# Performance work log

Measured on AMD Instinct MI355X. Metric: run time of the kernel, lower is better.

The kernel has to match this reference:

```python
import jax, jax.numpy as jnp
import numpy as np

D_MODEL = 1024
H = 16
D_K = D_MODEL // H
D_FF = 4096
EPS = 1e-6


def setup_inputs() -> dict:
    key = jax.random.key(0)
    ks = jax.random.split(key, 12)
    B, S = 8, 1024
    s = 0.02
    inp = {
        "x": jax.random.normal(ks[0], (B, S, D_MODEL), dtype=jnp.float32),
        "src_mask": jnp.ones((B, 1, 1, S), dtype=jnp.int32),
        "wq": jax.random.normal(ks[1], (D_MODEL, D_MODEL), dtype=jnp.float32) * s,
        "bq": jnp.zeros((D_MODEL,), jnp.float32),
        "wk": jax.random.normal(ks[2], (D_MODEL, D_MODEL), dtype=jnp.float32) * s,
        "bk": jnp.zeros((D_MODEL,), jnp.float32),
        "wv": jax.random.normal(ks[3], (D_MODEL, D_MODEL), dtype=jnp.float32) * s,
        "bv": jnp.zeros((D_MODEL,), jnp.float32),
        "wo": jax.random.normal(ks[4], (D_MODEL, D_MODEL), dtype=jnp.float32) * s,
        "bo": jnp.zeros((D_MODEL,), jnp.float32),
        "w1": jax.random.normal(ks[5], (D_FF, D_MODEL), dtype=jnp.float32) * s,
        "b1": jnp.zeros((D_FF,), jnp.float32),
        "w2": jax.random.normal(ks[6], (D_MODEL, D_FF), dtype=jnp.float32) * s,
        "b2": jnp.zeros((D_MODEL,), jnp.float32),
        "ln1_a": jnp.ones((1,), jnp.float32),
        "ln1_b": jnp.zeros((1,), jnp.float32),
        "ln2_a": jnp.ones((1,), jnp.float32),
        "ln2_b": jnp.zeros((1,), jnp.float32),
    }
    return inp


def _layernorm(x, alpha, bias):
    # matches torch: std with Bessel correction (ddof=1), eps added to std
    mean = jnp.mean(x, axis=-1, keepdims=True)
    std = jnp.std(x, axis=-1, keepdims=True, ddof=1)
    return (x - mean) / (std + EPS) * alpha + bias


def reference(x, src_mask, wq, bq, wk, bk, wv, bv, wo, bo, w1, b1, w2, b2,
              ln1_a, ln1_b, ln2_a, ln2_b):
    B, S, _ = x.shape
    # --- residual 1: self attention on pre-normed x ---
    n = _layernorm(x, ln1_a, ln1_b)
    q = n @ wq.T + bq
    # NOTE: the source has a bug: key and value are views of the *query*
    # projection (w_k/w_v outputs are computed but discarded). We reproduce it.
    _ = n @ wk.T + bk
    _ = n @ wv.T + bv
    qh = q.reshape(B, S, H, D_K).transpose(0, 2, 1, 3)  # [B,H,S,dk]
    kh = qh
    vh = qh
    scores = jnp.einsum('bhqd,bhkd->bhqk', qh, kh) / jnp.sqrt(jnp.float32(D_K))
    scores = jnp.where(src_mask == 0, jnp.float32(-1e9), scores)
    attn = jax.nn.softmax(scores, axis=-1)
    ctx = jnp.einsum('bhqk,bhkd->bhqd', attn, vh)
    ctx = ctx.transpose(0, 2, 1, 3).reshape(B, S, D_MODEL)
    x = x + (ctx @ wo.T + bo)
    # --- residual 2: feed-forward (intended ReLU MLP) ---
    n2 = _layernorm(x, ln2_a, ln2_b)
    h = jax.nn.relu(n2 @ w1.T + b1)
    x = x + (h @ w2.T + b2)
    return x
```

## Files before the change

### kernel.cpp

```cpp
#include <hip/hip_runtime.h>
#include <hip/hip_bf16.h>

typedef __attribute__((ext_vector_type(8))) short short8;
typedef __attribute__((ext_vector_type(4))) float f32x4;

#define MFMA16(a, b, c) __builtin_amdgcn_mfma_f32_16x16x32_bf16((a), (b), (c), 0, 0, 0)

__device__ __forceinline__ unsigned short f2bf(float f) {
  union { float f; unsigned int u; } v; v.f = f;
  return (unsigned short)((v.u + 0x7fffu + ((v.u >> 16) & 1u)) >> 16);
}

__device__ __forceinline__ void gload_lds16(const void* g, void* l) {
  __builtin_amdgcn_global_load_lds((__attribute__((address_space(1))) void*)g,
                                   (__attribute__((address_space(3))) void*)l,
                                   16, 0, 0);
}

struct CvtArgs {
  const float* s0; const float* s1; const float* s2; const float* s3;
  unsigned short* d0; unsigned short* d1; unsigned short* d2; unsigned short* d3;
};

__global__ __launch_bounds__(256) void cvt_weights(CvtArgs a) {
  const long N0 = 1048576, N1 = 1048576, N2 = 4194304;
  long i = ((long)blockIdx.x * 256 + threadIdx.x) * 4;
  const float* s; unsigned short* d; long off;
  if (i < N0)                { s = a.s0; d = a.d0; off = i; }
  else if (i < N0 + N1)      { s = a.s1; d = a.d1; off = i - N0; }
  else if (i < N0 + N1 + N2) { s = a.s2; d = a.d2; off = i - N0 - N1; }
  else                       { s = a.s3; d = a.d3; off = i - N0 - N1 - N2; }
  float4 v = *(const float4*)(s + off);
  ushort4 o;
  o.x = f2bf(v.x); o.y = f2bf(v.y); o.z = f2bf(v.z); o.w = f2bf(v.w);
  *(ushort4*)(d + off) = o;
}

__global__ __launch_bounds__(256) void ln_kernel(
    const float* __restrict__ x,
    const float* __restrict__ alpha, const float* __restrict__ beta,
    unsigned short* __restrict__ out) {
  const int row = blockIdx.x;
  const int tid = threadIdx.x;
  const float4 v = ((const float4*)(x + (size_t)row * 1024))[tid];
  float s  = v.x + v.y + v.z + v.w;
  float sq = v.x * v.x + v.y * v.y + v.z * v.z + v.w * v.w;
  #pragma unroll
  for (int d = 32; d >= 1; d >>= 1) {
    s  += __shfl_xor(s, d, 64);
    sq += __shfl_xor(sq, d, 64);
  }
  __shared__ float red[8];
  const int w = tid >> 6;
  if ((tid & 63) == 0) { red[w] = s; red[4 + w] = sq; }
  __syncthreads();
  s  = red[0] + red[1] + red[2] + red[3];
  sq = red[4] + red[5] + red[6] + red[7];
  const float mean = s * (1.f / 1024.f);
  float var = (sq - s * mean) * (1.f / 1023.f);
  var = fmaxf(var, 0.f);
  const float rs = alpha[0] / (sqrtf(var) + 1e-6f);
  const float bb = beta[0];
  ushort4 o;
  o.x = f2bf((v.x - mean) * rs + bb);
  o.y = f2bf((v.y - mean) * rs + bb);
  o.z = f2bf((v.z - mean) * rs + bb);
  o.w = f2bf((v.w - mean) * rs + bb);
  ((ushort4*)out)[(size_t)row * 256 + tid] = o;
}

template <int OUT_BF16, int RELU, int NF>
__global__ __launch_bounds__(512, 2) void gemm2ph(
    const unsigned short* __restrict__ A, int lda,
    const unsigned short* __restrict__ B, int ldb,
    const float* __restrict__ bias,
    const float* __restrict__ residual,
    void* __restrict__ Cout,
    int M, int N, int K, float cscale, int nbx) {
  __shared__ __align__(16) unsigned short lds[32768 + NF * 8192];
  const int NT = K >> 6;
  const int tid = threadIdx.x;
  const int w = tid >> 6, lane = tid & 63;
  const int cpx = gridDim.x >> 3;
  const int id = (blockIdx.x & 7) * cpx + (blockIdx.x >> 3);
  const int bx = id % nbx, by = id / nbx;
  const int row0 = by * 256, col0 = bx * (NF * 64);
  const int wr128 = (w >> 2) * 128, wcN = (w & 3) * (NF * 16);
  const int lq = lane & 15, g = lane >> 4, g4 = g * 4;
  const int strow = tid >> 3;
  const int sunit8 = ((tid & 7) ^ (strow & 7)) * 8;

  const unsigned short* Asrc = A + (size_t)(row0 + strow) * lda + sunit8;
  const unsigned short* Bsrc = B + (size_t)(col0 + strow) * ldb + sunit8;

  auto stage = [&](int buf, int tt) {
    unsigned short* Ad = lds + buf * 16384 + w * 512;
    unsigned short* Bd = lds + 32768 + buf * (NF * 4096) + w * 512;
    #pragma unroll
    for (int c = 0; c < 4; ++c)
      gload_lds16(Asrc + (size_t)(c * 64) * lda + tt * 64, Ad + c * 4096);
    #pragma unroll
    for (int c = 0; c < NF; ++c)
      gload_lds16(Bsrc + (size_t)(c * 64) * ldb + tt * 64, Bd + c * 4096);
  };

  f32x4 acc[8][NF] = {};

  stage(0, 0);
  asm volatile("s_waitcnt vmcnt(0)" ::: "memory");
  __builtin_amdgcn_s_barrier();
  int buf = 0;

  for (int t = 0; t < NT; ++t) {
    if (t + 1 < NT) stage(buf ^ 1, t + 1);
    const unsigned short* Ab = lds + buf * 16384;
    const unsigned short* Bb = lds + 32768 + buf * (NF * 4096);
    #pragma unroll
    for (int kk = 0; kk < 2; ++kk) {
      short8 af[8], bf[NF];
      #pragma unroll
      for (int m = 0; m < 8; ++m) {
        const int r = wr128 + m * 16 + lq;
        af[m] = *(const short8*)(Ab + r * 64 + (((kk * 4 + g) ^ (r & 7)) << 3));
      }
      #pragma unroll
      for (int n = 0; n < NF; ++n) {
        const int r = wcN + n * 16 + lq;
        bf[n] = *(const short8*)(Bb + r * 64 + (((kk * 4 + g) ^ (r & 7)) << 3));
      }
      __builtin_amdgcn_s_setprio(1);
      #pragma unroll
      for (int m = 0; m < 8; ++m)
        #pragma unroll
        for (int n = 0; n < NF; ++n)
          acc[m][n] = MFMA16(af[m], bf[n], acc[m][n]);
      __builtin_amdgcn_s_setprio(0);
    }
    if (t + 1 < NT) {
      asm volatile("s_waitcnt vmcnt(0)" ::: "memory");
      __builtin_amdgcn_s_barrier();
      buf ^= 1;
    }
  }

  float bv[NF];
  #pragma unroll
  for (int n = 0; n < NF; ++n) bv[n] = bias[col0 + wcN + n * 16 + lq];

  if (OUT_BF16) {
    const int CW = NF * 64 + 4;
    unsigned short* cbuf = lds;
    __syncthreads();
    #pragma unroll
    for (int p = 0; p < 2; ++p) {
      if ((w >> 2) == p) {
        #pragma unroll
        for (int m = 0; m < 8; ++m)
          #pragma unroll
          for (int n = 0; n < NF; ++n)
            #pragma unroll
            for (int r = 0; r < 4; ++r) {
              float v = (acc[m][n][r] + bv[n]) * cscale;
              if (RELU) v = fmaxf(v, 0.f);
              cbuf[(m * 16 + g4 + r) * CW + wcN + n * 16 + lq] = f2bf(v);
            }
      }
      __syncthreads();
      #pragma unroll
      for (int i = 0; i < 2 * NF; ++i) {
        const int un = i * 512 + tid;
        const int row = un / (8 * NF);
        const int cu = un % (8 * NF);
        const short8 vv = *(const short8*)&cbuf[row * CW + cu * 8];
        *(short8*)((unsigned short*)Cout + (size_t)(row0 + p * 128 + row) * N + col0 + cu * 8) = vv;
      }
      __syncthreads();
    }
  } else {
    #pragma unroll
    for (int n = 0; n < NF; ++n) {
      const int col = col0 + wcN + n * 16 + lq;
      #pragma unroll
      for (int m = 0; m < 8; ++m) {
        #pragma unroll
        for (int r = 0; r < 4; ++r) {
          const int row = row0 + wr128 + m * 16 + g4 + r;
          float v = (acc[m][n][r] + bv[n]) * cscale;
          if (RELU) v = fmaxf(v, 0.f);
          const size_t idx = (size_t)row * N + col;
          if (residual) v += residual[idx];
          ((float*)Cout)[idx] = v;
        }
      }
    }
  }
}

__global__ __launch_bounds__(256) void transpose_q(
    const unsigned short* __restrict__ q, unsigned short* __restrict__ qT) {
  const int st = blockIdx.x, bh = blockIdx.y;
  const int b = bh >> 4, h = bh & 15;
  __shared__ __align__(16) unsigned short tile[64][80];
  const int tid = threadIdx.x;
  const unsigned short* src = q + ((size_t)(b * 1024 + st * 64)) * 1024 + h * 64;
  #pragma unroll
  for (int j = 0; j < 2; ++j) {
    const int u = tid + j * 256;
    const int sl = u >> 3, d8 = (u & 7) * 8;
    *(short8*)&tile[sl][d8] = *(const short8*)&src[(size_t)sl * 1024 + d8];
  }
  __syncthreads();
  unsigned short* dst = qT + ((size_t)(bh * 64)) * 1024 + st * 64;
  #pragma unroll
  for (int j = 0; j < 2; ++j) {
    const int u = tid + j * 256;
    const int dl = u >> 3, s8 = (u & 7) * 8;
    short8 o;
    #pragma unroll
    for (int i = 0; i < 8; ++i) o[i] = (short)tile[s8 + i][dl];
    *(short8*)&dst[(size_t)dl * 1024 + s8] = o;
  }
}

__global__ __launch_bounds__(256) void attn_kernel(
    const unsigned short* __restrict__ q,
    const unsigned short* __restrict__ qT,
    const int* __restrict__ mask,
    unsigned short* __restrict__ ctx) {
  __shared__ __align__(16) unsigned short Ks[2][64 * 64];
  __shared__ __align__(16) unsigned short Vs[2][64 * 64];
  __shared__ int allmask;
  const int id = blockIdx.x;
  const int bh = ((id & 7) << 4) + (id >> 6);
  const int qt = (id >> 3) & 7;
  const int b = bh >> 4, h = bh & 15;
  const int tid = threadIdx.x, w = tid >> 6, lane = tid & 63;
  const int lq = lane & 15;
  const int g = lane >> 4;
  const int lk8 = g * 8;
  const int swz = lane & 7;
  const int q0 = qt * 128 + w * 32;
  const size_t qbase = (size_t)b * (1024 * 1024) + h * 64;
  const size_t qTb = (size_t)bh * 64 * 1024;
  const int srow = lane >> 3;
  const int su = (lane & 7) ^ srow;
  const size_t ksrc = qbase + (size_t)(w * 16 + srow) * 1024 + su * 8;
  const size_t vsrc = qTb + (size_t)(w * 16 + srow) * 1024 + su * 8;
  const float RS = 2.3548202f;

  auto stage = [&](int bufi, int kt) {
    char* Kd = (char*)Ks[bufi] + w * 2048;
    char* Vd = (char*)Vs[bufi] + w * 2048;
    gload_lds16(q + ksrc + (size_t)(kt * 64) * 1024, Kd);
    gload_lds16(q + ksrc + (size_t)(kt * 64 + 8) * 1024, Kd + 1024);
    gload_lds16(qT + vsrc + kt * 64, Vd);
    gload_lds16(qT + vsrc + (size_t)8 * 1024 + kt * 64, Vd + 1024);
  };

  const int* mrow = mask + b * 1024;
  if (tid == 0) allmask = 1;
  int mp = 1;
  #pragma unroll
  for (int i = 0; i < 4; ++i) mp &= (mrow[tid + i * 256] != 0);
  stage(0, 0);
  __syncthreads();
  if (!__all(mp) && lane == 0) atomicAnd(&allmask, 0);
  asm volatile("s_waitcnt vmcnt(0)" ::: "memory");
  __syncthreads();
  const bool fullmask = (allmask != 0);

  short8 qa[2][2];
  #pragma unroll
  for (int qf = 0; qf < 2; ++qf)
    #pragma unroll
    for (int kk = 0; kk < 2; ++kk)
      qa[qf][kk] = *(const short8*)&q[qbase + (size_t)(q0 + qf * 16 + lq) * 1024 + kk * 32 + lk8];

  short8 ones;
  #pragma unroll
  for (int i = 0; i < 8; ++i) ones[i] = (short)0x3F80;

  float mrun[2] = {-1e30f, -1e30f};
  f32x4 lacc[2] = {};
  f32x4 Oa[2][4];
  #pragma unroll
  for (int mf = 0; mf < 2; ++mf)
    #pragma unroll
    for (int nf = 0; nf < 4; ++nf) Oa[mf][nf] = (f32x4){0.f, 0.f, 0.f, 0.f};

  int cur = 0;

  for (int kt = 0; kt < 16; ++kt) {
    const int k0 = kt * 64;
    if (kt < 15) stage(cur ^ 1, kt + 1);
    const char* Kb = (const char*)Ks[cur];
    const char* Vb = (const char*)Vs[cur];
    f32x4 s[2][4];
    #pragma unroll
    for (int qf = 0; qf < 2; ++qf)
      #pragma unroll
      for (int kf = 0; kf < 4; ++kf) s[qf][kf] = (f32x4){0.f, 0.f, 0.f, 0.f};
    #pragma unroll
    for (int kf = 0; kf < 4; ++kf) {
      const char* kr = Kb + (kf * 16 + lq) * 128;
      const short8 ka0 = *(const short8*)(kr + (((g) ^ swz) << 4));
      const short8 ka1 = *(const short8*)(kr + (((4 + g) ^ swz) << 4));
      s[0][kf] = MFMA16(ka0, qa[0][0], s[0][kf]);
      s[0][kf] = MFMA16(ka1, qa[0][1], s[0][kf]);
      s[1][kf] = MFMA16(ka0, qa[1][0], s[1][kf]);
      s[1][kf] = MFMA16(ka1, qa[1][1], s[1][kf]);
    }
    float pmax[2] = {-1e30f, -1e30f};
    if (fullmask) {
      #pragma unroll
      for (int kf = 0; kf < 4; ++kf)
        #pragma unroll
        for (int qf = 0; qf < 2; ++qf)
          #pragma unroll
          for (int r = 0; r < 4; ++r)
            pmax[qf] = fmaxf(pmax[qf], s[qf][kf][r]);
    } else {
      #pragma unroll
      for (int kf = 0; kf < 4; ++kf) {
        const int4 mv = *(const int4*)&mrow[k0 + kf * 16 + g * 4];
        float madd[4];
        madd[0] = mv.x ? 0.f : -1e9f; madd[1] = mv.y ? 0.f : -1e9f;
        madd[2] = mv.z ? 0.f : -1e9f; madd[3] = mv.w ? 0.f : -1e9f;
        #pragma unroll
        for (int qf = 0; qf < 2; ++qf)
          #pragma unroll
          for (int r = 0; r < 4; ++r) {
            const float v = s[qf][kf][r] + madd[r];
            s[qf][kf][r] = v;
            pmax[qf] = fmaxf(pmax[qf], v);
          }
      }
    }
    #pragma unroll
    for (int qf = 0; qf < 2; ++qf) {
      pmax[qf] = fmaxf(pmax[qf], __shfl_xor(pmax[qf], 16, 64));
      pmax[qf] = fmaxf(pmax[qf], __shfl_xor(pmax[qf], 32, 64));
    }
    const int ok = (pmax[0] <= mrun[0] + 8.f) && (pmax[1] <= mrun[1] + 8.f);
    if (!__all(ok)) {
      float corr[2];
      #pragma unroll
      for (int qf = 0; qf < 2; ++qf) {
        const float mn = fmaxf(mrun[qf], pmax[qf]);
        corr[qf] = exp2f(mrun[qf] - mn);
        mrun[qf] = mn;
      }
      #pragma unroll
      for (int mf = 0; mf < 2; ++mf)
        #pragma unroll
        for (int r = 0; r < 4; ++r) {
          const float c = __shfl(corr[mf], g * 4 + r, 64);
          lacc[mf][r] *= c;
          #pragma unroll
          for (int nf = 0; nf < 4; ++nf) Oa[mf][nf][r] *= c;
        }
    }
    unsigned int E[2][4], O[2][4];
    #pragma unroll
    for (int qf = 0; qf < 2; ++qf) {
      #pragma unroll
      for (int kf = 0; kf < 4; ++kf) {
        float p0 = exp2f(s[qf][kf][0] - mrun[qf]);
        float p1 = exp2f(s[qf][kf][1] - mrun[qf]);
        float p2 = exp2f(s[qf][kf][2] - mrun[qf]);
        float p3 = exp2f(s[qf][kf][3] - mrun[qf]);
        asm("v_cvt_pk_bf16_f32 %0, %1, %2" : "=v"(E[qf][kf]) : "v"(p0), "v"(p1));
        asm("v_cvt_pk_bf16_f32 %0, %1, %2" : "=v"(O[qf][kf]) : "v"(p2), "v"(p3));
      }
    }
    short8 pa[2][2];
    #pragma unroll
    for (int qf = 0; qf < 2; ++qf) {
      #pragma unroll
      for (int ks = 0; ks < 2; ++ks) {
        unsigned int e0 = E[qf][2 * ks], e1 = E[qf][2 * ks + 1];
        unsigned int o0 = O[qf][2 * ks], o1 = O[qf][2 * ks + 1];
        asm("v_permlane32_swap_b32 %0, %1" : "+v"(e0), "+v"(e1));
        asm("v_permlane16_swap_b32 %0, %1" : "+v"(e0), "+v"(e1));
        asm("v_permlane32_swap_b32 %0, %1" : "+v"(o0), "+v"(o1));
        asm("v_permlane16_swap_b32 %0, %1" : "+v"(o0), "+v"(o1));
        union { unsigned int u[4]; short8 s8; } pw;
        pw.u[0] = e0; pw.u[1] = o0; pw.u[2] = e1; pw.u[3] = o1;
        pa[qf][ks] = pw.s8;
      }
    }
    #pragma unroll
    for (int ks = 0; ks < 2; ++ks) {
      #pragma unroll
      for (int nf = 0; nf < 4; ++nf) {
        const short8 vb = *(const short8*)(Vb + (nf * 16 + lq) * 128 + (((4 * ks + g) ^ swz) << 4));
        Oa[0][nf] = MFMA16(pa[0][ks], vb, Oa[0][nf]);
        Oa[1][nf] = MFMA16(pa[1][ks], vb, Oa[1][nf]);
      }
      lacc[0] = MFMA16(pa[0][ks], ones, lacc[0]);
      lacc[1] = MFMA16(pa[1][ks], ones, lacc[1]);
    }
    __syncthreads();
    cur ^= 1;
  }
  #pragma unroll
  for (int mf = 0; mf < 2; ++mf) {
    #pragma unroll
    for (int r = 0; r < 4; ++r) {
      const float linv = RS / lacc[mf][r];
      const int row = q0 + mf * 16 + g * 4 + r;
      #pragma unroll
      for (int nf = 0; nf < 4; ++nf) {
        const int col = h * 64 + nf * 16 + lq;
        ctx[((size_t)b * 1024 + row) * 1024 + col] = f2bf(Oa[mf][nf][r] * linv);
      }
    }
  }
}

extern "C" void kernel_launch(void* const* d_in, const int* in_sizes, int n_in,
                              void* d_out, int out_size, void* d_ws, size_t ws_size,
                              hipStream_t stream) {
  const float* x    = (const float*)d_in[0];
  const int*   mask = (const int*)d_in[1];
  const float* wq   = (const float*)d_in[2];
  const float* bq   = (const float*)d_in[3];
  const float* wo   = (const float*)d_in[8];
  const float* bo   = (const float*)d_in[9];
  const float* w1   = (const float*)d_in[10];
  const float* b1   = (const float*)d_in[11];
  const float* w2   = (const float*)d_in[12];
  const float* b2   = (const float*)d_in[13];
  const float* ln1a = (const float*)d_in[14];
  const float* ln1b = (const float*)d_in[15];
  const float* ln2a = (const float*)d_in[16];
  const float* ln2b = (const float*)d_in[17];
  float* out = (float*)d_out;

  char* ws = (char*)d_ws;
  unsigned short* wq_b  = (unsigned short*)(ws);
  unsigned short* wo_b  = (unsigned short*)(ws + (2l << 20));
  unsigned short* w1_b  = (unsigned short*)(ws + (4l << 20));
  unsigned short* w2_b  = (unsigned short*)(ws + (12l << 20));
  unsigned short* n_b   = (unsigned short*)(ws + (20l << 20));
  unsigned short* q_b   = (unsigned short*)(ws + (36l << 20));
  unsigned short* qT_b  = (unsigned short*)(ws + (52l << 20));
  unsigned short* ctx_b = (unsigned short*)(ws + (68l << 20));
  unsigned short* h_b   = (unsigned short*)(ws + (84l << 20));

  const float SQRT_SC = 0.42466090f;

  CvtArgs ca{wq, wo, w1, w2, wq_b, wo_b, w1_b, w2_b};
  cvt_weights<<<10240, 256, 0, stream>>>(ca);
  ln_kernel<<<8192, 256, 0, stream>>>(x, ln1a, ln1b, n_b);
  gemm2ph<1, 0, 2><<<256, 512, 0, stream>>>(n_b, 1024, wq_b, 1024, bq, nullptr, q_b, 8192, 1024, 1024, SQRT_SC, 8);
  transpose_q<<<dim3(16, 128), 256, 0, stream>>>(q_b, qT_b);
  attn_kernel<<<1024, 256, 0, stream>>>(q_b, qT_b, mask, ctx_b);
  gemm2ph<0, 0, 2><<<256, 512, 0, stream>>>(ctx_b, 1024, wo_b, 1024, bo, x, out, 8192, 1024, 1024, 1.0f, 8);
  ln_kernel<<<8192, 256, 0, stream>>>(out, ln2a, ln2b, n_b);
  gemm2ph<1, 1, 4><<<512, 512, 0, stream>>>(n_b, 1024, w1_b, 1024, b1, nullptr, h_b, 8192, 4096, 1024, 1.0f, 16);
  gemm2ph<0, 0, 2><<<256, 512, 0, stream>>>(h_b, 4096, w2_b, 4096, b2, out, out, 8192, 1024, 4096, 1.0f, 8);
}
```

Before: 323.4 us.

## Switch GEMMs to triple-buffered LDS pipeline with fixed 256x128 tiles

Replaces the double-buffered GEMM with a three-stage LDS ring: two tiles are prefetched ahead, and each iteration waits only on the older outstanding loads (vmcnt(6)) instead of draining all of them. The tile width is fixed at 128 columns, so the FFN up-projection now uses 256x128 tiles across 1024 blocks instead of 256x256 tiles across 512. LDS use rises to about 144KB per block and launch bounds drop to one block per CU. Hiding more global-load latency comes at the cost of occupancy and less B-tile reuse in the wide GEMM.

```diff
diff --git a/kernel.cpp b/kernel.cpp
--- a/kernel.cpp
+++ b/kernel.cpp
@@ -69,23 +69,23 @@
   ((ushort4*)out)[(size_t)row * 256 + tid] = o;
 }
 
-template <int OUT_BF16, int RELU, int NF>
-__global__ __launch_bounds__(512, 2) void gemm2ph(
+template <int OUT_BF16, int RELU>
+__global__ __launch_bounds__(512, 1) void gemm3(
     const unsigned short* __restrict__ A, int lda,
     const unsigned short* __restrict__ B, int ldb,
     const float* __restrict__ bias,
     const float* __restrict__ residual,
     void* __restrict__ Cout,
     int M, int N, int K, float cscale, int nbx) {
-  __shared__ __align__(16) unsigned short lds[32768 + NF * 8192];
+  __shared__ __align__(16) unsigned short lds[3 * 24576];
   const int NT = K >> 6;
   const int tid = threadIdx.x;
   const int w = tid >> 6, lane = tid & 63;
   const int cpx = gridDim.x >> 3;
   const int id = (blockIdx.x & 7) * cpx + (blockIdx.x >> 3);
   const int bx = id % nbx, by = id / nbx;
-  const int row0 = by * 256, col0 = bx * (NF * 64);
-  const int wr128 = (w >> 2) * 128, wcN = (w & 3) * (NF * 16);
+  const int row0 = by * 256, col0 = bx * 128;
+  const int wr128 = (w >> 2) * 128, wcN = (w & 3) * 32;
   const int lq = lane & 15, g = lane >> 4, g4 = g * 4;
   const int strow = tid >> 3;
   const int sunit8 = ((tid & 7) ^ (strow & 7)) * 8;
@@ -93,38 +93,46 @@
   const unsigned short* Asrc = A + (size_t)(row0 + strow) * lda + sunit8;
   const unsigned short* Bsrc = B + (size_t)(col0 + strow) * ldb + sunit8;
 
-  auto stage = [&](int buf, int tt) {
-    unsigned short* Ad = lds + buf * 16384 + w * 512;
-    unsigned short* Bd = lds + 32768 + buf * (NF * 4096) + w * 512;
+  auto stage = [&](int bufi, int tt) {
+    unsigned short* Ad = lds + bufi * 24576 + w * 512;
+    unsigned short* Bd = lds + bufi * 24576 + 16384 + w * 512;
     #pragma unroll
     for (int c = 0; c < 4; ++c)
       gload_lds16(Asrc + (size_t)(c * 64) * lda + tt * 64, Ad + c * 4096);
     #pragma unroll
-    for (int c = 0; c < NF; ++c)
+    for (int c = 0; c < 2; ++c)
       gload_lds16(Bsrc + (size_t)(c * 64) * ldb + tt * 64, Bd + c * 4096);
   };
 
-  f32x4 acc[8][NF] = {};
+  f32x4 acc[8][2] = {};
 
   stage(0, 0);
-  asm volatile("s_waitcnt vmcnt(0)" ::: "memory");
+  if (NT > 1) {
+    stage(1, 1);
+    asm volatile("s_waitcnt vmcnt(6)" ::: "memory");
+  } else {
+    asm volatile("s_waitcnt vmcnt(0)" ::: "memory");
+  }
   __builtin_amdgcn_s_barrier();
-  int buf = 0;
+  int cur = 0;
 
   for (int t = 0; t < NT; ++t) {
-    if (t + 1 < NT) stage(buf ^ 1, t + 1);
-    const unsigned short* Ab = lds + buf * 16384;
-    const unsigned short* Bb = lds + 32768 + buf * (NF * 4096);
+    if (t + 2 < NT) {
+      int stg = cur + 2; if (stg >= 3) stg -= 3;
+      stage(stg, t + 2);
+    }
+    const unsigned short* Ab = lds + cur * 24576;
+    const unsigned short* Bb = lds + cur * 24576 + 16384;
     #pragma unroll
     for (int kk = 0; kk < 2; ++kk) {
-      short8 af[8], bf[NF];
+      short8 af[8], bf[2];
       #pragma unroll
       for (int m = 0; m < 8; ++m) {
         const int r = wr128 + m * 16 + lq;
         af[m] = *(const short8*)(Ab + r * 64 + (((kk * 4 + g) ^ (r & 7)) << 3));
       }
       #pragma unroll
-      for (int n = 0; n < NF; ++n) {
+      for (int n = 0; n < 2; ++n) {
         const int r = wcN + n * 16 + lq;
         bf[n] = *(const short8*)(Bb + r * 64 + (((kk * 4 + g) ^ (r & 7)) << 3));
       }
@@ -132,23 +140,24 @@
       #pragma unroll
       for (int m = 0; m < 8; ++m)
         #pragma unroll
-        for (int n = 0; n < NF; ++n)
+        for (int n = 0; n < 2; ++n)
           acc[m][n] = MFMA16(af[m], bf[n], acc[m][n]);
       __builtin_amdgcn_s_setprio(0);
     }
     if (t + 1 < NT) {
-      asm volatile("s_waitcnt vmcnt(0)" ::: "memory");
+      if (t + 2 < NT) asm volatile("s_waitcnt vmcnt(6)" ::: "memory");
+      else            asm volatile("s_waitcnt vmcnt(0)" ::: "memory");
       __builtin_amdgcn_s_barrier();
-      buf ^= 1;
-    }
-  }
-
-  float bv[NF];
-  #pragma unroll
-  for (int n = 0; n < NF; ++n) bv[n] = bias[col0 + wcN + n * 16 + lq];
+      cur = (cur == 2) ? 0 : cur + 1;
+    }
+  }
+
+  float bv[2];
+  #pragma unroll
+  for (int n = 0; n < 2; ++n) bv[n] = bias[col0 + wcN + n * 16 + lq];
 
   if (OUT_BF16) {
-    const int CW = NF * 64 + 4;
+    const int CW = 132;
     unsigned short* cbuf = lds;
     __syncthreads();
     #pragma unroll
@@ -157,7 +166,7 @@
         #pragma unroll
         for (int m = 0; m < 8; ++m)
           #pragma unroll
-          for (int n = 0; n < NF; ++n)
+          for (int n = 0; n < 2; ++n)
             #pragma unroll
             for (int r = 0; r < 4; ++r) {
               float v = (acc[m][n][r] + bv[n]) * cscale;
@@ -167,10 +176,10 @@
       }
       __syncthreads();
       #pragma unroll
-      for (int i = 0; i < 2 * NF; ++i) {
+      for (int i = 0; i < 4; ++i) {
         const int un = i * 512 + tid;
-        const int row = un / (8 * NF);
-        const int cu = un % (8 * NF);
+        const int row = un >> 4;
+        const int cu = un & 15;
         const short8 vv = *(const short8*)&cbuf[row * CW + cu * 8];
         *(short8*)((unsigned short*)Cout + (size_t)(row0 + p * 128 + row) * N + col0 + cu * 8) = vv;
       }
@@ -178,7 +187,7 @@
     }
   } else {
     #pragma unroll
-    for (int n = 0; n < NF; ++n) {
+    for (int n = 0; n < 2; ++n) {
       const int col = col0 + wcN + n * 16 + lq;
       #pragma unroll
       for (int m = 0; m < 8; ++m) {
@@ -453,11 +462,11 @@
   CvtArgs ca{wq, wo, w1, w2, wq_b, wo_b, w1_b, w2_b};
   cvt_weights<<<10240, 256, 0, stream>>>(ca);
   ln_kernel<<<8192, 256, 0, stream>>>(x, ln1a, ln1b, n_b);
-  gemm2ph<1, 0, 2><<<256, 512, 0, stream>>>(n_b, 1024, wq_b, 1024, bq, nullptr, q_b, 8192, 1024, 1024, SQRT_SC, 8);
+  gemm3<1, 0><<<256, 512, 0, stream>>>(n_b, 1024, wq_b, 1024, bq, nullptr, q_b, 8192, 1024, 1024, SQRT_SC, 8);
   transpose_q<<<dim3(16, 128), 256, 0, stream>>>(q_b, qT_b);
   attn_kernel<<<1024, 256, 0, stream>>>(q_b, qT_b, mask, ctx_b);
-  gemm2ph<0, 0, 2><<<256, 512, 0, stream>>>(ctx_b, 1024, wo_b, 1024, bo, x, out, 8192, 1024, 1024, 1.0f, 8);
+  gemm3<0, 0><<<256, 512, 0, stream>>>(ctx_b, 1024, wo_b, 1024, bo, x, out, 8192, 1024, 1024, 1.0f, 8);
   ln_kernel<<<8192, 256, 0, stream>>>(out, ln2a, ln2b, n_b);
-  gemm2ph<1, 1, 4><<<512, 512, 0, stream>>>(n_b, 1024, w1_b, 1024, b1, nullptr, h_b, 8192, 4096, 1024, 1.0f, 16);
-  gemm2ph<0, 0, 2><<<256, 512, 0, stream>>>(h_b, 4096, w2_b, 4096, b2, out, out, 8192, 1024, 4096, 1.0f, 8);
-}
+  gemm3<1, 1><<<1024, 512, 0, stream>>>(n_b, 1024, w1_b, 1024, b1, nullptr, h_b, 8192, 4096, 1024, 1.0f, 32);
+  gemm3<0, 0><<<256, 512, 0, stream>>>(h_b, 4096, w2_b, 4096, b2, out, out, 8192, 1024, 4096, 1.0f, 8);
+}
```

Result: slower. 340.9 us (+5.4%).
